# Kernel tuning notes

Measured on AMD Instinct MI355X. Metric: run time of the kernel, lower is better.

Reference implementation:

```python
import jax, jax.numpy as jnp
import numpy as np

B = 4096
FEAT = 512
EMB = 64
HID = 1024
NUM_CLASSES = 64   # == option_num == noise_lib_Y.shape[0]
LIB_X = 256
LIB_Y = 256
OUT_J = 256


def setup_inputs() -> dict:
    key = jax.random.key(0)
    ks = jax.random.split(key, 16)
    s = lambda k, shape, fan: jax.random.normal(k, shape, jnp.float32) / np.sqrt(fan)
    d_in = FEAT + EMB
    return {
        "state": jax.random.normal(ks[0], (B, FEAT), jnp.float32),
        "option": jax.random.randint(ks[1], (B,), 0, NUM_CLASSES, jnp.int64),
        "embed_table": s(ks[2], (NUM_CLASSES, EMB), EMB),
        "Wx1": s(ks[3], (d_in, HID), d_in), "bx1": jnp.zeros((HID,), jnp.float32),
        "Wx2": s(ks[4], (HID, LIB_X), HID), "bx2": jnp.zeros((LIB_X,), jnp.float32),
        "Wy1": s(ks[5], (d_in, HID), d_in), "by1": jnp.zeros((HID,), jnp.float32),
        "Wy2": s(ks[6], (HID, LIB_Y), HID), "by2": jnp.zeros((LIB_Y,), jnp.float32),
        "noise_lib_X": s(ks[7], (LIB_X, OUT_J), LIB_X),
        "noise_lib_Y": s(ks[8], (NUM_CLASSES, LIB_Y, OUT_J), LIB_Y),
    }


def _mlp(x, W1, b1, W2, b2):
    # MLP_RELU, layer_num=2: Linear -> ReLU -> Linear
    h = jax.nn.relu(x @ W1 + b1)
    return h @ W2 + b2


def reference(state, option, embed_table, Wx1, bx1, Wx2, bx2,
              Wy1, by1, Wy2, by2, noise_lib_X, noise_lib_Y):
    option_embed = embed_table[option]                      # [B, EMB]
    all_state = jnp.concatenate([state, option_embed], axis=-1)
    cls_X = _mlp(all_state, Wx1, bx1, Wx2, bx2)             # [B, LIB_X]
    cls_Y = _mlp(all_state, Wy1, by1, Wy2, by2)             # [B, LIB_Y]
    # Original: einsum('bi,mij->bmj') then mask with one_hot(option).
    # Mathematically identical gather-then-matmul (honors the routing sparsity):
    noise_Y_sel = noise_lib_Y[option]                       # [B, LIB_Y, OUT_J]
    generate_noise_Y = jnp.einsum('bi,bij->bj', cls_Y, noise_Y_sel)
    generate_noise_X = cls_X @ noise_lib_X                  # [B, OUT_J]
    return (generate_noise_X, generate_noise_Y)
```

## Files before the change

### kernel.cpp

```cpp
#include <hip/hip_runtime.h>

typedef unsigned short u16;
typedef unsigned int u32;

using f32x4  = __attribute__((ext_vector_type(4))) float;
using bf16x8 = __attribute__((ext_vector_type(8))) __bf16;

#define DEV __device__ __forceinline__

DEV u16 f2bf(float f) {
  union { float f; u32 u; } x; x.f = f;
  return (u16)((x.u + 0x7fffu + ((x.u >> 16) & 1u)) >> 16);
}
DEV float bf2f(u16 h) {
  union { u32 u; float f; } x; x.u = ((u32)h) << 16;
  return x.f;
}

DEV void async_cp16(const u16* g, u16* l) {
  __builtin_amdgcn_global_load_lds((const __attribute__((address_space(1))) void*)g,
                                   (__attribute__((address_space(3))) void*)l,
                                   16, 0, 0);
}

static constexpr int BATCH = 4096;
static constexpr int FEAT  = 512;
static constexpr int EMB   = 64;
static constexpr int HID   = 1024;
static constexpr int NC    = 64;
static constexpr int DIN   = 576;
static constexpr int LIB   = 256;

DEV void detect_lite(const u32* __restrict__ sraw, const u32* __restrict__ oraw,
                     int* isf32, int* ostr) {
  __shared__ int cib, conz;
  const int t = threadIdx.x;
  if (t == 0) { cib = 0; conz = 0; }
  u32 w = sraw[t];
  u32 e = (w >> 7) & 0xFFu;
  unsigned long long m1 = __ballot(e >= 100 && e <= 142);
  unsigned long long m2 = __ballot((t & 1) && oraw[t] != 0);
  __syncthreads();
  if ((t & 63) == 0) {
    atomicAdd(&cib, __popcll(m1));
    atomicAdd(&conz, __popcll(m2));
  }
  __syncthreads();
  *isf32 = (cib < 128) ? 1 : 0;
  *ostr  = (conz == 0) ? 2 : 1;
}

DEV void load16_bf(u16* v, const void* __restrict__ in, size_t off, int isf32) {
  if (isf32) {
    const float4* s = (const float4*)((const float*)in + off);
    float4 a0 = s[0], a1 = s[1], a2 = s[2], a3 = s[3];
    v[0] = f2bf(a0.x); v[1] = f2bf(a0.y); v[2]  = f2bf(a0.z); v[3]  = f2bf(a0.w);
    v[4] = f2bf(a1.x); v[5] = f2bf(a1.y); v[6]  = f2bf(a1.z); v[7]  = f2bf(a1.w);
    v[8] = f2bf(a2.x); v[9] = f2bf(a2.y); v[10] = f2bf(a2.z); v[11] = f2bf(a2.w);
    v[12] = f2bf(a3.x); v[13] = f2bf(a3.y); v[14] = f2bf(a3.z); v[15] = f2bf(a3.w);
  } else {
    const uint4* s = (const uint4*)((const u16*)in + off);
    *(uint4*)&v[0] = s[0];
    *(uint4*)&v[8] = s[1];
  }
}

DEV void do_transpose64(u16* lds, const void* __restrict__ in,
                        u16* __restrict__ out, int R, int C,
                        int by, int bx, int isf32) {
  u16* tile = lds;
  const int t = threadIdx.x;
  {
    const int r = t >> 2, c0 = (t & 3) * 16;
    u16 v[16];
    load16_bf(v, in, (size_t)(by * 64 + r) * C + (bx * 64 + c0), isf32);
    *(uint4*)&tile[r * 72 + c0]     = *(uint4*)&v[0];
    *(uint4*)&tile[r * 72 + c0 + 8] = *(uint4*)&v[8];
  }
  __syncthreads();
  {
    const int c = t & 63, rs = (t >> 6) * 16;
    u16 w[16];
#pragma unroll
    for (int i = 0; i < 16; ++i) w[i] = tile[(rs + i) * 72 + c];
    size_t oo = (size_t)(bx * 64 + c) * R + (by * 64 + rs);
    *(uint4*)&out[oo]     = *(uint4*)&w[0];
    *(uint4*)&out[oo + 8] = *(uint4*)&w[8];
  }
}

DEV void tgemm_task(u16* lds, const void* __restrict__ nX,
                    const void* __restrict__ Wx2, u16* __restrict__ T,
                    int mt, int nt, int isf32) {
  u16* Als = lds;
  u16* Bls = lds + 64 * 72;
  const int t = threadIdx.x;
  const int m0 = mt * 64, q0 = nt * 64;
  const int lane = t & 63, wid = t >> 6;
  const int wm = wid >> 1, wn = wid & 1;
  const int lr = lane & 15, lq = lane >> 4;
  f32x4 acc[2][2] = {};
  for (int k0 = 0; k0 < LIB; k0 += 64) {
    __syncthreads();
    {
      const int r = t >> 2, c0 = (t & 3) * 16;
      u16 v[16];
      load16_bf(v, nX, (size_t)(k0 + r) * LIB + m0 + c0, isf32);
#pragma unroll
      for (int j = 0; j < 16; ++j) Als[(c0 + j) * 72 + r] = v[j];
      const int q = t >> 2, ic = (t & 3) * 16;
      u16 w16[16];
      load16_bf(w16, Wx2, (size_t)(q0 + q) * LIB + k0 + ic, isf32);
      u16* dst = &Bls[((ic >> 5) * 64 + q) * 32 + (ic & 31)];
      *(uint4*)dst       = *(uint4*)&w16[0];
      *(uint4*)(dst + 8) = *(uint4*)&w16[8];
    }
    __syncthreads();
#pragma unroll
    for (int sl = 0; sl < 2; ++sl) {
      bf16x8 av[2], bv[2];
#pragma unroll
      for (int i2 = 0; i2 < 2; ++i2)
        av[i2] = *(const bf16x8*)&Als[(wm * 32 + i2 * 16 + lr) * 72 + sl * 32 + lq * 8];
#pragma unroll
      for (int j2 = 0; j2 < 2; ++j2)
        bv[j2] = *(const bf16x8*)&Bls[(sl * 64 + wn * 32 + j2 * 16 + lr) * 32 + lq * 8];
#pragma unroll
      for (int i2 = 0; i2 < 2; ++i2)
#pragma unroll
        for (int j2 = 0; j2 < 2; ++j2)
          acc[i2][j2] = __builtin_amdgcn_mfma_f32_16x16x32_bf16(av[i2], bv[j2], acc[i2][j2], 0, 0, 0);
    }
  }
#pragma unroll
  for (int j2 = 0; j2 < 2; ++j2) {
    const int gc = q0 + wn * 32 + j2 * 16 + lr;
#pragma unroll
    for (int i2 = 0; i2 < 2; ++i2) {
      const int gr = m0 + wm * 32 + i2 * 16 + lq * 4;
#pragma unroll
      for (int r = 0; r < 4; ++r)
        T[(size_t)(gr + r) * HID + gc] = f2bf(acc[i2][j2][r]);
    }
  }
}

struct PrepArgs {
  const void *state, *emb, *Wx1, *Wy1, *Wy2, *Wx2, *nX, *bx2;
  const int* opt;
  u16 *all_state, *WT1x, *WT1y, *WT2y, *T;
  float* b2x;
};
static constexpr int PB_CONCAT = BATCH * 36 / 256;
static constexpr int PB_WT1 = (DIN / 64) * (HID / 64);
static constexpr int PB_WT2 = (HID / 64) * (LIB / 64);
static constexpr int PB_TG  = (LIB / 64) * (HID / 64);
static constexpr int PB_BIAS = 4;
static constexpr int PREP_BLOCKS = PB_CONCAT + 2 * PB_WT1 + PB_WT2 + PB_TG
                                 + PB_BIAS;

__global__ __launch_bounds__(256) void prep_k(PrepArgs a) {
  __shared__ __align__(16) u16 plds[64 * 72 + 128 * 32];
  __shared__ float red[4][64];
  int isf32, os;
  detect_lite((const u32*)a.state, (const u32*)a.opt, &isf32, &os);
  int bid = blockIdx.x;
  const int t = threadIdx.x;
  if (bid < PB_CONCAT) {
    int idx = bid * 256 + t;
    int b = idx / 36, ch = idx % 36;
    const void* base;
    size_t srcoff;
    if (ch < 32) { base = a.state; srcoff = (size_t)b * FEAT + ch * 16; }
    else {
      base = a.emb;
      srcoff = (size_t)a.opt[(size_t)b * os] * EMB + (ch - 32) * 16;
    }
    u16 o[16];
    load16_bf(o, base, srcoff, isf32);
    u16* dst = a.all_state + (size_t)b * DIN + ch * 16;
    *(uint4*)dst       = *(const uint4*)&o[0];
    *(uint4*)(dst + 8) = *(const uint4*)&o[8];
    return;
  }
  bid -= PB_CONCAT;
  if (bid < PB_WT1) { do_transpose64(plds, a.Wx1, a.WT1x, DIN, HID, bid >> 4, bid & 15, isf32); return; }
  bid -= PB_WT1;
  if (bid < PB_WT1) { do_transpose64(plds, a.Wy1, a.WT1y, DIN, HID, bid >> 4, bid & 15, isf32); return; }
  bid -= PB_WT1;
  if (bid < PB_WT2) { do_transpose64(plds, a.Wy2, a.WT2y, HID, LIB, bid >> 2, bid & 3, isf32); return; }
  bid -= PB_WT2;
  if (bid < PB_TG) { tgemm_task(plds, a.nX, a.Wx2, a.T, bid & 3, bid >> 2, isf32); return; }
  bid -= PB_TG;
  {
    const int j = bid * 64 + (t & 63), g = t >> 6;
    float acc = 0.f;
    for (int ii = 0; ii < 64; ++ii) {
      const int i = g * 64 + ii;
      float s = isf32 ? ((const float*)a.bx2)[i] : bf2f(((const u16*)a.bx2)[i]);
      float v = isf32 ? ((const float*)a.nX)[(size_t)i * LIB + j]
                      : bf2f(((const u16*)a.nX)[(size_t)i * LIB + j]);
      acc += s * v;
    }
    red[g][t & 63] = acc;
    __syncthreads();
    if (g == 0)
      a.b2x[j] = red[0][t & 63] + red[1][t & 63] + red[2][t & 63] + red[3][t & 63];
  }
}

template <int BM, int BN, bool RELU>
DEV void gemm_tile(u16* lds, const u16* __restrict__ A, const u16* __restrict__ Bt,
                   const void* bias, void* C, int N, int K, int m0, int n0,
                   int isf32, bool cf32, bool bf32) {
  constexpr int WM = BM / 2, WN = BN / 2, TM = WM / 16, TN = WN / 16;
  u16* As = lds;
  u16* Bs = lds + BM * 64;
  const int t = threadIdx.x;
  const int lane = t & 63, wid = t >> 6;
  const int wm = wid >> 1, wn = wid & 1;
  const int lr = lane & 15, lq = lane >> 4;
  f32x4 acc[TM][TN] = {};
  for (int k0 = 0; k0 < K; k0 += 64) {
    __syncthreads();
#pragma unroll
    for (int sl = 0; sl < 2; ++sl) {
#pragma unroll
      for (int u = 0; u < BM / 64; ++u) {
        int unit = u * 256 + t;
        int r = unit >> 2, c8 = (unit & 3) * 8;
        async_cp16(A + (size_t)(m0 + r) * K + (k0 + sl * 32 + c8),
                   &As[(sl * BM + r) * 32 + c8]);
      }
#pragma unroll
      for (int u = 0; u < BN / 64; ++u) {
        int unit = u * 256 + t;
        int r = unit >> 2, c8 = (unit & 3) * 8;
        async_cp16(Bt + (size_t)(n0 + r) * K + (k0 + sl * 32 + c8),
                   &Bs[(sl * BN + r) * 32 + c8]);
      }
    }
    __syncthreads();
#pragma unroll
    for (int sl = 0; sl < 2; ++sl) {
      bf16x8 av[TM], bv[TN];
#pragma unroll
      for (int i = 0; i < TM; ++i)
        av[i] = *(const bf16x8*)&As[(sl * BM + wm * WM + i * 16 + lr) * 32 + lq * 8];
#pragma unroll
      for (int j = 0; j < TN; ++j)
        bv[j] = *(const bf16x8*)&Bs[(sl * BN + wn * WN + j * 16 + lr) * 32 + lq * 8];
#pragma unroll
      for (int i = 0; i < TM; ++i)
#pragma unroll
        for (int j = 0; j < TN; ++j)
          acc[i][j] = __builtin_amdgcn_mfma_f32_16x16x32_bf16(av[i], bv[j], acc[i][j], 0, 0, 0);
    }
  }
#pragma unroll
  for (int j = 0; j < TN; ++j) {
    const int gc = n0 + wn * WN + j * 16 + lr;
    const float bval = bias
        ? (bf32 ? ((const float*)bias)[gc] : bf2f(((const u16*)bias)[gc]))
        : 0.f;
#pragma unroll
    for (int i = 0; i < TM; ++i) {
      const int gr = m0 + wm * WM + i * 16 + lq * 4;
#pragma unroll
      for (int r = 0; r < 4; ++r) {
        float v = acc[i][j][r] + bval;
        if (RELU) v = fmaxf(v, 0.f);
        const size_t idx = (size_t)(gr + r) * N + gc;
        if (cf32) ((float*)C)[idx] = v;
        else      ((u16*)C)[idx] = f2bf(v);
      }
    }
  }
}

struct GArg { const u16* A; const u16* Bt; const void* bias; void* C; int cflag; int bflag; };

template <int BM, int BN, bool RELU>
__global__ __launch_bounds__(256) void gemm_bt(GArg g0, GArg g1, int N, int K,
                                               const void* state, const void* opt) {
  __shared__ __align__(16) u16 lds[(BM + BN) * 64];
  int isf32, os;
  detect_lite((const u32*)state, (const u32*)opt, &isf32, &os);
  const GArg g = blockIdx.z ? g1 : g0;
  gemm_tile<BM, BN, RELU>(lds, g.A, g.Bt, g.bias, g.C, N, K,
                          blockIdx.y * BM, blockIdx.x * BN,
                          isf32, g.cflag && isf32, g.bflag || isf32);
}

struct TailArgs {
  const u16* cls_y;
  const void *nY, *state;
  const int* opt;
  void* out;
};

__global__ __launch_bounds__(256) void tail_k(TailArgs a) {
  __shared__ __align__(16) u16 lds[25216];
  __shared__ int wcnt[4], lbase;
  int isf32, os;
  detect_lite((const u32*)a.state, (const u32*)a.opt, &isf32, &os);
  const bool of32 = (isf32 != 0);
  const int t = threadIdx.x;
  const int lane = t & 63, w = t >> 6, lr = lane & 15, lq = lane >> 4;

  u16* Bts  = lds;
  u16* Asm  = lds + 16896;
  u16* list = lds + 21120;
  const int m = blockIdx.x >> 2, n0 = (blockIdx.x & 3) * 64;

#pragma unroll
  for (int pass = 0; pass < 4; ++pass) {
    const int k = pass * 64 + (t >> 2), nc = (t & 3) * 16;
    u16 v[16];
    load16_bf(v, a.nY, ((size_t)m * LIB + k) * LIB + n0 + nc, isf32);
#pragma unroll
    for (int j = 0; j < 16; ++j) Bts[(nc + j) * 264 + k] = v[j];
  }

  if (t == 0) lbase = 0;
  __syncthreads();
  for (int base = 0; base < BATCH; base += 256) {
    const int b = base + t;
    const int e = a.opt[(size_t)b * os];
    unsigned long long mk = __ballot(e == m);
    if (lane == 0) wcnt[w] = __popcll(mk);
    __syncthreads();
    int wpre = lbase;
    for (int i = 0; i < w; ++i) wpre += wcnt[i];
    const int mypre = __popcll(mk & ((1ull << lane) - 1ull));
    if (e == m) list[wpre + mypre] = (u16)b;
    __syncthreads();
    if (t == 0) lbase += wcnt[0] + wcnt[1] + wcnt[2] + wcnt[3];
  }
  __syncthreads();
  const int cnt = lbase;
  const size_t out_off = (size_t)BATCH * LIB;

  for (int ch = 0; ch < cnt; ch += 16) {
    __syncthreads();
    {
      const int r = t >> 4, cb = (t & 15) * 16;
      if (ch + r < cnt) {
        const u16* src = a.cls_y + (size_t)list[ch + r] * LIB + cb;
        *(uint4*)&Asm[r * 264 + cb]     = *(const uint4*)src;
        *(uint4*)&Asm[r * 264 + cb + 8] = *(const uint4*)(src + 8);
      } else {
        uint4 z{0, 0, 0, 0};
        *(uint4*)&Asm[r * 264 + cb]     = z;
        *(uint4*)&Asm[r * 264 + cb + 8] = z;
      }
    }
    __syncthreads();
    f32x4 acc = {};
#pragma unroll
    for (int kk = 0; kk < LIB; kk += 32) {
      bf16x8 av = *(const bf16x8*)&Asm[lr * 264 + kk + lq * 8];
      bf16x8 bv = *(const bf16x8*)&Bts[(w * 16 + lr) * 264 + kk + lq * 8];
      acc = __builtin_amdgcn_mfma_f32_16x16x32_bf16(av, bv, acc, 0, 0, 0);
    }
#pragma unroll
    for (int r = 0; r < 4; ++r) {
      const int rowc = lq * 4 + r;
      if (ch + rowc < cnt) {
        const size_t oi = out_off + (size_t)list[ch + rowc] * LIB
                        + (n0 + w * 16 + lr);
        if (of32) ((float*)a.out)[oi] = acc[r];
        else      ((u16*)a.out)[oi] = f2bf(acc[r]);
      }
    }
  }
}

extern "C" void kernel_launch(void* const* d_in, const int* in_sizes, int n_in,
                              void* d_out, int out_size, void* d_ws, size_t ws_size,
                              hipStream_t stream) {
  char* p = (char*)d_ws;
  auto alloc = [&](size_t bytes) { char* r = p; p += (bytes + 255) & ~(size_t)255; return r; };
  u16* all_state = (u16*)alloc((size_t)BATCH * DIN * 2);
  u16* h_x   = (u16*)alloc((size_t)BATCH * HID * 2);
  u16* h_y   = (u16*)alloc((size_t)BATCH * HID * 2);
  u16* cls_y = (u16*)alloc((size_t)BATCH * LIB * 2);
  u16* WT1x  = (u16*)alloc((size_t)HID * DIN * 2);
  u16* WT1y  = (u16*)alloc((size_t)HID * DIN * 2);
  u16* WT2y  = (u16*)alloc((size_t)LIB * HID * 2);
  u16* T     = (u16*)alloc((size_t)LIB * HID * 2);
  float* b2x = (float*)alloc((size_t)LIB * 4);

  const void* state = d_in[0];
  const void* opt   = d_in[1];

  PrepArgs pa;
  pa.state = state; pa.opt = (const int*)opt; pa.emb = d_in[2];
  pa.Wx1 = d_in[3]; pa.Wx2 = d_in[5]; pa.bx2 = d_in[6];
  pa.Wy1 = d_in[7]; pa.Wy2 = d_in[9]; pa.nX = d_in[11];
  pa.all_state = all_state; pa.WT1x = WT1x; pa.WT1y = WT1y; pa.WT2y = WT2y;
  pa.T = T; pa.b2x = b2x;
  prep_k<<<PREP_BLOCKS, 256, 0, stream>>>(pa);

  GArg g1x{all_state, WT1x, d_in[4], h_x, 0, 0};
  GArg g1y{all_state, WT1y, d_in[8], h_y, 0, 0};
  gemm_bt<128, 128, true><<<dim3(HID / 128, BATCH / 128, 2), 256, 0, stream>>>(
      g1x, g1y, HID, DIN, state, opt);

  GArg g2x{h_x, T, b2x, d_out, 1, 1};
  GArg g2y{h_y, WT2y, d_in[10], cls_y, 0, 0};
  gemm_bt<64, 64, false><<<dim3(LIB / 64, BATCH / 64, 2), 256, 0, stream>>>(
      g2x, g2y, LIB, HID, state, opt);

  TailArgs ta{cls_y, d_in[12], state, (const int*)opt, d_out};
  tail_k<<<256, 256, 0, stream>>>(ta);
}
```

Measured before the change: 155.3 us.

## Move T-gemm and bias folding into first GEMM launch, remap block order

```diff
diff --git a/kernel.cpp b/kernel.cpp
--- a/kernel.cpp
+++ b/kernel.cpp
@@ -146,22 +146,17 @@
 }
 
 struct PrepArgs {
-  const void *state, *emb, *Wx1, *Wy1, *Wy2, *Wx2, *nX, *bx2;
+  const void *state, *emb, *Wx1, *Wy1, *Wy2;
   const int* opt;
-  u16 *all_state, *WT1x, *WT1y, *WT2y, *T;
-  float* b2x;
+  u16 *all_state, *WT1x, *WT1y, *WT2y;
 };
 static constexpr int PB_CONCAT = BATCH * 36 / 256;
 static constexpr int PB_WT1 = (DIN / 64) * (HID / 64);
 static constexpr int PB_WT2 = (HID / 64) * (LIB / 64);
-static constexpr int PB_TG  = (LIB / 64) * (HID / 64);
-static constexpr int PB_BIAS = 4;
-static constexpr int PREP_BLOCKS = PB_CONCAT + 2 * PB_WT1 + PB_WT2 + PB_TG
-                                 + PB_BIAS;
+static constexpr int PREP_BLOCKS = PB_CONCAT + 2 * PB_WT1 + PB_WT2;
 
 __global__ __launch_bounds__(256) void prep_k(PrepArgs a) {
-  __shared__ __align__(16) u16 plds[64 * 72 + 128 * 32];
-  __shared__ float red[4][64];
+  __shared__ __align__(16) u16 plds[64 * 72];
   int isf32, os;
   detect_lite((const u32*)a.state, (const u32*)a.opt, &isf32, &os);
   int bid = blockIdx.x;
@@ -188,25 +183,7 @@
   bid -= PB_WT1;
   if (bid < PB_WT1) { do_transpose64(plds, a.Wy1, a.WT1y, DIN, HID, bid >> 4, bid & 15, isf32); return; }
   bid -= PB_WT1;
-  if (bid < PB_WT2) { do_transpose64(plds, a.Wy2, a.WT2y, HID, LIB, bid >> 2, bid & 3, isf32); return; }
-  bid -= PB_WT2;
-  if (bid < PB_TG) { tgemm_task(plds, a.nX, a.Wx2, a.T, bid & 3, bid >> 2, isf32); return; }
-  bid -= PB_TG;
-  {
-    const int j = bid * 64 + (t & 63), g = t >> 6;
-    float acc = 0.f;
-    for (int ii = 0; ii < 64; ++ii) {
-      const int i = g * 64 + ii;
-      float s = isf32 ? ((const float*)a.bx2)[i] : bf2f(((const u16*)a.bx2)[i]);
-      float v = isf32 ? ((const float*)a.nX)[(size_t)i * LIB + j]
-                      : bf2f(((const u16*)a.nX)[(size_t)i * LIB + j]);
-      acc += s * v;
-    }
-    red[g][t & 63] = acc;
-    __syncthreads();
-    if (g == 0)
-      a.b2x[j] = red[0][t & 63] + red[1][t & 63] + red[2][t & 63] + red[3][t & 63];
-  }
+  do_transpose64(plds, a.Wy2, a.WT2y, HID, LIB, bid >> 2, bid & 3, isf32);
 }
 
 template <int BM, int BN, bool RELU>
@@ -275,6 +252,52 @@
         else      ((u16*)C)[idx] = f2bf(v);
       }
     }
+  }
+}
+
+struct G1Args {
+  const u16 *all_state, *WT1x, *WT1y;
+  const void *bx1, *by1, *nX, *Wx2, *bx2, *state, *opt;
+  u16 *h_x, *h_y, *T;
+  float* b2x;
+};
+
+__global__ __launch_bounds__(256) void gemm1_k(G1Args a) {
+  __shared__ __align__(16) u16 lds[256 * 64];
+  __shared__ float red[4][64];
+  int isf32, os;
+  detect_lite((const u32*)a.state, (const u32*)a.opt, &isf32, &os);
+  const int g = blockIdx.x, t = threadIdx.x;
+  if (g < 512) {
+    const int c = g & 7;
+    const int head = c & 1;
+    const int n = (c >> 1) | (((g >> 3) & 1) << 2);
+    const int m = g >> 4;
+    gemm_tile<128, 128, true>(lds,
+        a.all_state, head ? a.WT1y : a.WT1x, head ? a.by1 : a.bx1,
+        head ? a.h_y : a.h_x, HID, DIN, m * 128, n * 128, isf32, false, isf32);
+    return;
+  }
+  if (g < 576) {
+    const int id = g - 512;
+    tgemm_task(lds, a.nX, a.Wx2, a.T, id & 3, id >> 2, isf32);
+    return;
+  }
+  {
+    const int bid = g - 576;
+    const int j = bid * 64 + (t & 63), grp = t >> 6;
+    float acc = 0.f;
+    for (int ii = 0; ii < 64; ++ii) {
+      const int i = grp * 64 + ii;
+      float s = isf32 ? ((const float*)a.bx2)[i] : bf2f(((const u16*)a.bx2)[i]);
+      float v = isf32 ? ((const float*)a.nX)[(size_t)i * LIB + j]
+                      : bf2f(((const u16*)a.nX)[(size_t)i * LIB + j]);
+      acc += s * v;
+    }
+    red[grp][t & 63] = acc;
+    __syncthreads();
+    if (grp == 0)
+      a.b2x[j] = red[0][t & 63] + red[1][t & 63] + red[2][t & 63] + red[3][t & 63];
   }
 }
 
@@ -396,16 +419,17 @@
 
   PrepArgs pa;
   pa.state = state; pa.opt = (const int*)opt; pa.emb = d_in[2];
-  pa.Wx1 = d_in[3]; pa.Wx2 = d_in[5]; pa.bx2 = d_in[6];
-  pa.Wy1 = d_in[7]; pa.Wy2 = d_in[9]; pa.nX = d_in[11];
+  pa.Wx1 = d_in[3]; pa.Wy1 = d_in[7]; pa.Wy2 = d_in[9];
   pa.all_state = all_state; pa.WT1x = WT1x; pa.WT1y = WT1y; pa.WT2y = WT2y;
-  pa.T = T; pa.b2x = b2x;
   prep_k<<<PREP_BLOCKS, 256, 0, stream>>>(pa);
 
-  GArg g1x{all_state, WT1x, d_in[4], h_x, 0, 0};
-  GArg g1y{all_state, WT1y, d_in[8], h_y, 0, 0};
-  gemm_bt<128, 128, true><<<dim3(HID / 128, BATCH / 128, 2), 256, 0, stream>>>(
-      g1x, g1y, HID, DIN, state, opt);
+  G1Args g1;
+  g1.all_state = all_state; g1.WT1x = WT1x; g1.WT1y = WT1y;
+  g1.bx1 = d_in[4]; g1.by1 = d_in[8];
+  g1.nX = d_in[11]; g1.Wx2 = d_in[5]; g1.bx2 = d_in[6];
+  g1.state = state; g1.opt = opt;
+  g1.h_x = h_x; g1.h_y = h_y; g1.T = T; g1.b2x = b2x;
+  gemm1_k<<<580, 256, 0, stream>>>(g1);
 
   GArg g2x{h_x, T, b2x, d_out, 1, 1};
   GArg g2y{h_y, WT2y, d_in[10], cls_y, 0, 0};
```

New measurement: 157.1 us. Within noise of the previous version (+1.2%).
